# Kernel tuning notes

Hardware: AMD Instinct MI355X
Metric: run time of the kernel (lower is better)

## Reference

```python
import jax, jax.numpy as jnp
import numpy as np
import math

B, S, D, H = 2, 2048, 1024, 16
DH = D // H  # head_dim = 64
NEG = -10000.0


def setup_inputs() -> dict:
    key = jax.random.key(0)
    ks = jax.random.split(key, 6)
    scale = 1.0 / math.sqrt(D)
    inp = {
        "query": jax.random.normal(ks[0], (B, S, D), dtype=jnp.float32),
        "key": jax.random.normal(ks[1], (B, S, D), dtype=jnp.float32),
        "value": jax.random.normal(ks[2], (B, S, D), dtype=jnp.float32),
        "Wq": jax.random.normal(ks[3], (D, D), dtype=jnp.float32) * scale,
        "Wk": jax.random.normal(ks[4], (D, D), dtype=jnp.float32) * scale,
        "Wv": jax.random.normal(ks[5], (D, D), dtype=jnp.float32) * scale,
        "pad_mask": jnp.ones((B, 1, 1, S), dtype=jnp.int32),
        "attn_mask": jnp.tril(jnp.ones((S, S), dtype=jnp.int32))[None, None],  # causal [1,1,S,S]
    }
    return inp


def reference(query, key, value, Wq, Wk, Wv, pad_mask, attn_mask):
    b, s, d = query.shape
    # torch Linear(bias=False): y = x @ W.T ; then split into heads [B,H,S,DH]
    def proj(x, W):
        return (x @ W.T).reshape(b, -1, H, DH).transpose(0, 2, 1, 3)

    Q = proj(query, Wq)
    K = proj(key, Wk)
    V = proj(value, Wv)

    scores = jnp.einsum("bhqd,bhkd->bhqk", Q, K) / math.sqrt(DH)
    scores = jnp.where(attn_mask == 0, NEG, scores)
    scores = jnp.where(pad_mask == 0, NEG, scores)
    attn = jax.nn.softmax(scores, axis=-1)  # dropout p=0.0 -> identity
    ctx = jnp.einsum("bhqk,bhkd->bhqd", attn, V)
    return ctx.transpose(0, 2, 1, 3).reshape(b, -1, d)
```

## Files before the change

### kernel.cpp

```cpp
#include <hip/hip_runtime.h>


typedef unsigned short u16;
typedef unsigned int u32;
typedef u16 u16x4 __attribute__((ext_vector_type(4)));
typedef u16 u16x8 __attribute__((ext_vector_type(8)));
typedef u32 u32x2 __attribute__((ext_vector_type(2)));
typedef u32 u32x4 __attribute__((ext_vector_type(4)));
typedef __bf16 bf16x8 __attribute__((ext_vector_type(8)));
typedef float f32x4 __attribute__((ext_vector_type(4)));

static __device__ __forceinline__ u16 f2bf(float f) {
  unsigned u = __builtin_bit_cast(unsigned, f);
  return (u16)((u + 0x7FFFu + ((u >> 16) & 1u)) >> 16);
}

static __device__ __forceinline__ u32 cvt_pk_bf16(float lo, float hi) {
  u32 r;
  asm("v_cvt_pk_bf16_f32 %0, %1, %2" : "=v"(r) : "v"(lo), "v"(hi));
  return r;
}

static __device__ __forceinline__ u16x8 cvt8(float4 f0, float4 f1) {
  u32x4 v;
  v[0] = cvt_pk_bf16(f0.x, f0.y);
  v[1] = cvt_pk_bf16(f0.z, f0.w);
  v[2] = cvt_pk_bf16(f1.x, f1.y);
  v[3] = cvt_pk_bf16(f1.z, f1.w);
  return __builtin_bit_cast(u16x8, v);
}

static __device__ __forceinline__ f32x4 mfma16(u16x8 a, u16x8 b, f32x4 c) {
  return __builtin_amdgcn_mfma_f32_16x16x32_bf16(
      __builtin_bit_cast(bf16x8, a), __builtin_bit_cast(bf16x8, b), c, 0, 0, 0);
}

static __device__ __forceinline__ float bperm_f(int lane, float v) {
  return __builtin_bit_cast(
      float, __builtin_amdgcn_ds_bpermute(lane * 4, __builtin_bit_cast(int, v)));
}

#define GLOAD16(GSRC, LDST)                                                  \
  __builtin_amdgcn_global_load_lds(                                         \
      (const __attribute__((address_space(1))) unsigned int*)(GSRC),        \
      (__attribute__((address_space(3))) unsigned int*)(LDST), 16, 0, 0)

#define FENCE() asm volatile("" ::: "memory")
#define BARX()                        \
  do {                                \
    __builtin_amdgcn_s_barrier();     \
    FENCE();                          \
  } while (0)

__global__ __launch_bounds__(256) void cvt_kernel(
    const float* __restrict__ Xq, const float* __restrict__ Xk,
    const float* __restrict__ Xv, const float* __restrict__ Wq,
    const float* __restrict__ Wk, const float* __restrict__ Wv,
    u16* __restrict__ Xb, u16* __restrict__ Wb) {
  const int y = blockIdx.y;
  const float* src = (y == 0) ? Xq : (y == 1) ? Xk : (y == 2) ? Xv
                   : (y == 3) ? Wq : (y == 4) ? Wk : Wv;
  const size_t nelem = (y < 3) ? (size_t)4 * 1024 * 1024 : (size_t)1024 * 1024;
  u16* dst = (y < 3) ? Xb + (size_t)y * 4 * 1024 * 1024
                     : Wb + (size_t)(y - 3) * 1024 * 1024;
  const size_t i = ((size_t)blockIdx.x * 256 + threadIdx.x) * 8;
  if (i >= nelem) return;
  const float4 f0 = *(const float4*)(src + i);
  const float4 f1 = *(const float4*)(src + i + 4);
  *(u16x8*)(dst + i) = cvt8(f0, f1);
}

__global__ __launch_bounds__(256) void proj_kernel(
    const u16* __restrict__ Xbf, const u16* __restrict__ Wbf,
    u16* __restrict__ Qb, u16* __restrict__ Kb, u16* __restrict__ Vt) {
  const int d0 = blockIdx.x;
  const int tid = (d0 & 7) * 96 + (d0 >> 3);
  const int nI = tid % 24, mI = tid / 24;
  const int mode = nI >> 3;
  const int m0 = mI * 128;
  const int n0 = (nI & 7) * 128;

  const u16* __restrict__ X = Xbf + (size_t)mode * (4 * 1024 * 1024);
  const u16* __restrict__ W = Wbf + (size_t)mode * (1024 * 1024);

  __shared__ __align__(16) char As[3][128 * 64];
  __shared__ __align__(16) char Bs[3][128 * 64];

  const int t = threadIdx.x;
  const int lane = t & 63;
  const int w = t >> 6;
  const int wm = w >> 1, wn = w & 1;
  const int lr = lane & 15, lg = lane >> 4;

  const u16* aptr[2];
  const u16* bptr[2];
  int soff[2];
#pragma unroll
  for (int jj = 0; jj < 2; ++jj) {
    const int j = w * 2 + jj;
    const int row = j * 16 + (lane >> 2);
    const int col = (lane & 3) * 8;
    aptr[jj] = X + (size_t)(m0 + row) * 1024 + col;
    bptr[jj] = W + (size_t)(n0 + row) * 1024 + col;
    soff[jj] = j * 1024;
  }

#define ISSUE(T, BUF)                                                \
  do {                                                               \
    _Pragma("unroll") for (int jj = 0; jj < 2; ++jj)                 \
        GLOAD16(aptr[jj] + (size_t)(T) * 32, As[BUF] + soff[jj]);    \
    _Pragma("unroll") for (int jj = 0; jj < 2; ++jj)                 \
        GLOAD16(bptr[jj] + (size_t)(T) * 32, Bs[BUF] + soff[jj]);    \
  } while (0)

  f32x4 acc[4][4] = {};

#define CMP(BUF)                                                              \
  do {                                                                       \
    u16x8 af[4], bfr[4];                                                     \
    _Pragma("unroll") for (int mi = 0; mi < 4; ++mi) {                        \
      const int row = wm * 64 + mi * 16 + lr;                                \
      af[mi] = *(const u16x8*)(As[BUF] + row * 64 + lg * 16);                \
    }                                                                         \
    _Pragma("unroll") for (int ni = 0; ni < 4; ++ni) {                        \
      const int row = wn * 64 + ni * 16 + lr;                                \
      bfr[ni] = *(const u16x8*)(Bs[BUF] + row * 64 + lg * 16);               \
    }                                                                         \
    _Pragma("unroll") for (int mi = 0; mi < 4; ++mi)                          \
        _Pragma("unroll") for (int ni = 0; ni < 4; ++ni)                      \
            acc[mi][ni] = mfma16(af[mi], bfr[ni], acc[mi][ni]);               \
  } while (0)

  ISSUE(0, 0);
  ISSUE(1, 1);
  ISSUE(2, 2);
  asm volatile("s_waitcnt vmcnt(8)" ::: "memory");
  BARX();

  for (int tt = 0; tt < 29; ++tt) {
    CMP(tt % 3);
    asm volatile("s_waitcnt lgkmcnt(0)" ::: "memory");
    BARX();
    ISSUE(tt + 3, tt % 3);
    asm volatile("s_waitcnt vmcnt(8)" ::: "memory");
    BARX();
  }
  CMP(29 % 3);
  asm volatile("s_waitcnt vmcnt(4)" ::: "memory");
  BARX();
  CMP(30 % 3);
  asm volatile("s_waitcnt vmcnt(0)" ::: "memory");
  BARX();
  CMP(31 % 3);
#undef ISSUE
#undef CMP

#pragma unroll
  for (int mi = 0; mi < 4; ++mi) {
    const int sbase = m0 + wm * 64 + mi * 16 + lg * 4;
    const int b_ = sbase >> 11;
    const int s_ = sbase & 2047;
#pragma unroll
    for (int ni = 0; ni < 4; ++ni) {
      const int n = n0 + wn * 64 + ni * 16 + lr;
      const int h_ = n >> 6, dh = n & 63;
      if (mode == 2) {
        u16x4 pk;
        pk[0] = f2bf(acc[mi][ni][0]);
        pk[1] = f2bf(acc[mi][ni][1]);
        pk[2] = f2bf(acc[mi][ni][2]);
        pk[3] = f2bf(acc[mi][ni][3]);
        *(u16x4*)(Vt + ((size_t)((b_ * 16 + h_) * 64 + dh)) * 2048 + s_) = pk;
      } else {
        const float sc = (mode == 0) ? 0.18033688f : 1.0f;
        u16* dst = (mode == 0 ? Qb : Kb) + (size_t)(b_ * 16 + h_) * (2048 * 64) + dh;
#pragma unroll
        for (int r = 0; r < 4; ++r)
          dst[(size_t)(s_ + r) * 64] = f2bf(acc[mi][ni][r] * sc);
      }
    }
  }
}

__global__ __launch_bounds__(256, 2) void attn_kernel(
    const u16* __restrict__ Qb, const u16* __restrict__ Kb, const u16* __restrict__ Vt,
    const int* __restrict__ pad, float* __restrict__ out) {
  const int id = blockIdx.x;
  const int g = id >> 8, r_ = id & 255;
  const int bh = r_ & 31;
  const int p8 = r_ >> 5;
  const int pi = g ? (15 - p8) : p8;
  const int qbA = 31 - pi, qbB = pi;

  const int b = bh >> 4, h = bh & 15;
  const u16* Qh = Qb + (size_t)bh * (2048 * 64);
  const u16* Kh = Kb + (size_t)bh * (2048 * 64);
  const u16* Vh = Vt + (size_t)bh * (64 * 2048);
  const int* padb = pad + b * 2048;

  __shared__ u16 Ks[2][64 * 64];
  __shared__ u16 Vs[2][64 * 64];
  __shared__ u16 Ps[4][16 * 64];

  const int t = threadIdx.x, lane = t & 63, w = t >> 6;
  const int lr = lane & 15, lg = lane >> 4;
  const int swz = (lr & 7) << 4;
  const int sr = t >> 3, scb = t & 7;
  const int qwaveA = qbA * 64 + w * 16, qwaveB = qbB * 64 + w * 16;

  u16x8 qfA[2], qfB[2];
#pragma unroll
  for (int kc = 0; kc < 2; ++kc) {
    qfA[kc] = *(const u16x8*)(Qh + (size_t)(qwaveA + lr) * 64 + kc * 32 + lg * 8);
    qfB[kc] = *(const u16x8*)(Qh + (size_t)(qwaveB + lr) * 64 + kc * 32 + lg * 8);
  }

  f32x4 accA[4] = {}, accB[4] = {};
  float mrowA = -1e4f, lsumA = 0.f, mrowB = -1e4f, lsumB = 0.f;

  u16x8 kr0, kr1, vr0, vr1;
  const int sb0 = (sr * 128 + scb * 16) ^ ((sr & 7) << 4);
  const int sb1 = ((32 + sr) * 128 + scb * 16) ^ ((sr & 7) << 4);

  kr0 = *(const u16x8*)(Kh + (size_t)sr * 64 + scb * 8);
  kr1 = *(const u16x8*)(Kh + (size_t)(32 + sr) * 64 + scb * 8);
  vr0 = *(const u16x8*)(Vh + (size_t)sr * 2048 + scb * 8);
  vr1 = *(const u16x8*)(Vh + (size_t)(32 + sr) * 2048 + scb * 8);
  *(u16x8*)((char*)Ks[0] + sb0) = kr0;
  *(u16x8*)((char*)Ks[0] + sb1) = kr1;
  *(u16x8*)((char*)Vs[0] + sb0) = vr0;
  *(u16x8*)((char*)Vs[0] + sb1) = vr1;
  __syncthreads();

#define PROCESS(QF, ACC, MROW, LSUM, QWAVE)                                    \
  do {                                                                         \
    f32x4 s4[4] = {};                                                          \
    __builtin_amdgcn_s_setprio(1);                                             \
    _Pragma("unroll") for (int ct = 0; ct < 4; ++ct) {                         \
      if (kv0 + ct * 16 <= (QWAVE) + 15) {                                     \
        _Pragma("unroll") for (int kc = 0; kc < 2; ++kc) {                     \
          const int byt = ((ct * 16 + lr) * 128 + kc * 64 + lg * 16) ^ swz;    \
          const u16x8 kf = *(const u16x8*)((char*)KsC + byt);                  \
          s4[ct] = mfma16(kf, QF[kc], s4[ct]);                                 \
        }                                                                      \
      }                                                                        \
    }                                                                          \
    __builtin_amdgcn_s_setprio(0);                                             \
    float vv[4][4];                                                            \
    if ((kv0 + 63 <= (QWAVE)) && allpad) {                                     \
      _Pragma("unroll") for (int ct = 0; ct < 4; ++ct)                         \
          _Pragma("unroll") for (int rr = 0; rr < 4; ++rr)                     \
              vv[ct][rr] = s4[ct][rr];                                         \
    } else {                                                                   \
      const int lim = (QWAVE) + lr - kv0 - lg * 4;                             \
      _Pragma("unroll") for (int ct = 0; ct < 4; ++ct) {                       \
        const int* pvp = (const int*)&pv4[ct];                                 \
        _Pragma("unroll") for (int rr = 0; rr < 4; ++rr)                       \
            vv[ct][rr] = (pvp[rr] && (ct * 16 + rr) <= lim) ? s4[ct][rr]       \
                                                            : -1e4f;           \
      }                                                                        \
    }                                                                          \
    float m0_ = fmaxf(fmaxf(fmaxf(vv[0][0], vv[0][1]), fmaxf(vv[0][2], vv[0][3])), \
                      fmaxf(fmaxf(vv[1][0], vv[1][1]), fmaxf(vv[1][2], vv[1][3]))); \
    float m1_ = fmaxf(fmaxf(fmaxf(vv[2][0], vv[2][1]), fmaxf(vv[2][2], vv[2][3])), \
                      fmaxf(fmaxf(vv[3][0], vv[3][1]), fmaxf(vv[3][2], vv[3][3]))); \
    float mx = fmaxf(m0_, m1_);                                                \
    mx = fmaxf(mx, __shfl_xor(mx, 16));                                        \
    mx = fmaxf(mx, __shfl_xor(mx, 32));                                        \
    if (!__all(mx <= (MROW) + 8.0f)) { \
      const float mn = fmaxf((MROW), mx);                                      \
      const float al = exp2f((MROW) - mn);                                     \
      (MROW) = mn;                                                             \
      (LSUM) *= al;                                                            \
      _Pragma("unroll") for (int rr = 0; rr < 4; ++rr) {                       \
        const float alv = bperm_f(lg * 4 + rr, al);                            \
        _Pragma("unroll") for (int dt = 0; dt < 4; ++dt) ACC[dt][rr] *= alv;   \
      }                                                                        \
    }                                                                          \
    float p[4][4];                                                             \
    _Pragma("unroll") for (int ct = 0; ct < 4; ++ct)                           \
        _Pragma("unroll") for (int rr = 0; rr < 4; ++rr)                       \
            p[ct][rr] = exp2f(vv[ct][rr] - (MROW));                            \
    float ps = (((p[0][0] + p[0][1]) + (p[0][2] + p[0][3])) +                  \
                ((p[1][0] + p[1][1]) + (p[1][2] + p[1][3]))) +                 \
               (((p[2][0] + p[2][1]) + (p[2][2] + p[2][3])) +                  \
                ((p[3][0] + p[3][1]) + (p[3][2] + p[3][3])));                  \
    ps += __shfl_xor(ps, 16);                                                  \
    ps += __shfl_xor(ps, 32);                                                  \
    (LSUM) += ps;                                                              \
    u16* PsB = &Ps[w][0];                                                      \
    _Pragma("unroll") for (int ct = 0; ct < 4; ++ct) {                         \
      u32x2 pw;                                                                \
      pw[0] = cvt_pk_bf16(p[ct][0], p[ct][1]);                                 \
      pw[1] = cvt_pk_bf16(p[ct][2], p[ct][3]);                                 \
      const int pb = (lr * 128 + ct * 32 + lg * 8) ^ swz;                      \
      *(u32x2*)((char*)PsB + pb) = pw;                                         \
    }                                                                          \
    const u16x8 pa0 = *(const u16x8*)((char*)PsB + ((lr * 128 + lg * 16) ^ swz));      \
    const u16x8 pa1 = *(const u16x8*)((char*)PsB + ((lr * 128 + 64 + lg * 16) ^ swz)); \
    __builtin_amdgcn_s_setprio(1);                                             \
    _Pragma("unroll") for (int dt = 0; dt < 4; ++dt) {                         \
      const int r0 = (dt * 16 + lr) * 128;                                     \
      ACC[dt] = mfma16(pa0, *(const u16x8*)((char*)VsC + ((r0 + lg * 16) ^ swz)), ACC[dt]);      \
      ACC[dt] = mfma16(pa1, *(const u16x8*)((char*)VsC + ((r0 + 64 + lg * 16) ^ swz)), ACC[dt]); \
    }                                                                          \
    __builtin_amdgcn_s_setprio(0);                                             \
  } while (0)

  int cur = 0;
  const int nst = qbA + 1;
  for (int st = 0; st < nst; ++st) {
    const int kv0 = st << 6;
    const bool more = st + 1 < nst;
    if (more) {
      const int nv0 = kv0 + 64;
      kr0 = *(const u16x8*)(Kh + (size_t)(nv0 + sr) * 64 + scb * 8);
      kr1 = *(const u16x8*)(Kh + (size_t)(nv0 + 32 + sr) * 64 + scb * 8);
      vr0 = *(const u16x8*)(Vh + (size_t)sr * 2048 + nv0 + scb * 8);
      vr1 = *(const u16x8*)(Vh + (size_t)(32 + sr) * 2048 + nv0 + scb * 8);
    }
    int4 pv4[4];
#pragma unroll
    for (int ct = 0; ct < 4; ++ct)
      pv4[ct] = *(const int4*)(padb + kv0 + ct * 16 + lg * 4);
    const int pall = pv4[0].x & pv4[0].y & pv4[0].z & pv4[0].w &
                     pv4[1].x & pv4[1].y & pv4[1].z & pv4[1].w &
                     pv4[2].x & pv4[2].y & pv4[2].z & pv4[2].w &
                     pv4[3].x & pv4[3].y & pv4[3].z & pv4[3].w;
    const bool allpad = __all(pall != 0);

    const u16* KsC = Ks[cur];
    const u16* VsC = Vs[cur];

    PROCESS(qfA, accA, mrowA, lsumA, qwaveA);
    if (st <= qbB)
      PROCESS(qfB, accB, mrowB, lsumB, qwaveB);

    if (more) {
      u16* Kn = Ks[cur ^ 1];
      u16* Vn = Vs[cur ^ 1];
      *(u16x8*)((char*)Kn + sb0) = kr0;
      *(u16x8*)((char*)Kn + sb1) = kr1;
      *(u16x8*)((char*)Vn + sb0) = vr0;
      *(u16x8*)((char*)Vn + sb1) = vr1;
    }
    __syncthreads();
    cur ^= 1;
  }
#undef PROCESS

#pragma unroll
  for (int tile = 0; tile < 2; ++tile) {
    const f32x4* acc = tile ? accB : accA;
    const float lsum = tile ? lsumB : lsumA;
    const int qwave = tile ? qwaveB : qwaveA;
    const float il = 1.0f / lsum;
    float* obase = out + ((size_t)(b * 2048 + qwave + lg * 4)) * 1024 + h * 64 + lr;
#pragma unroll
    for (int r = 0; r < 4; ++r) {
      const float linv = bperm_f(lg * 4 + r, il);
#pragma unroll
      for (int dt = 0; dt < 4; ++dt)
        obase[(size_t)r * 1024 + dt * 16] = acc[dt][r] * linv;
    }
  }
}

extern "C" void kernel_launch(void* const* d_in, const int* in_sizes, int n_in,
                              void* d_out, int out_size, void* d_ws, size_t ws_size,
                              hipStream_t stream) {
  const float* q  = (const float*)d_in[0];
  const float* k  = (const float*)d_in[1];
  const float* v  = (const float*)d_in[2];
  const float* wq = (const float*)d_in[3];
  const float* wk = (const float*)d_in[4];
  const float* wv = (const float*)d_in[5];
  const int* pad  = (const int*)d_in[6];
  float* out = (float*)d_out;

  u16* Qb  = (u16*)d_ws;
  u16* Kb  = Qb + (size_t)4 * 1024 * 1024;
  u16* Vt  = Kb + (size_t)4 * 1024 * 1024;
  u16* Wbf = Vt + (size_t)4 * 1024 * 1024;
  u16* Xbf = Wbf + (size_t)3 * 1024 * 1024;

  dim3 gv(2048, 6);
  cvt_kernel<<<gv, 256, 0, stream>>>(q, k, v, wq, wk, wv, Xbf, Wbf);

  proj_kernel<<<768, 256, 0, stream>>>(Xbf, Wbf, Qb, Kb, Vt);

  attn_kernel<<<512, 256, 0, stream>>>(Qb, Kb, Vt, pad, out);
}
```

Measured before the change: 106.0 us.

## Assign each wave 32 rows of one query tile, sharing K/V fragments

Work is split differently across waves. Before, each wave handled 16 rows of both query tiles. Now waves 0-1 take 32 rows of tile A and waves 2-3 take 32 rows of tile B, processing two 16-row groups together. Each K and V fragment read from LDS then feeds two MFMAs, roughly halving LDS traffic per unit of work, and the P scratch buffer doubles to 8 slices. The cost is load imbalance under the causal mask: the tile-B waves go idle once their tile is finished, while the tile-A waves carry double work on the critical path.

```diff
diff --git a/kernel.cpp b/kernel.cpp
--- a/kernel.cpp
+++ b/kernel.cpp
@@ -200,23 +200,26 @@
 
   __shared__ u16 Ks[2][64 * 64];
   __shared__ u16 Vs[2][64 * 64];
-  __shared__ u16 Ps[4][16 * 64];
+  __shared__ u16 Ps[8][16 * 64];
 
   const int t = threadIdx.x, lane = t & 63, w = t >> 6;
   const int lr = lane & 15, lg = lane >> 4;
   const int swz = (lr & 7) << 4;
   const int sr = t >> 3, scb = t & 7;
-  const int qwaveA = qbA * 64 + w * 16, qwaveB = qbB * 64 + w * 16;
-
-  u16x8 qfA[2], qfB[2];
-#pragma unroll
-  for (int kc = 0; kc < 2; ++kc) {
-    qfA[kc] = *(const u16x8*)(Qh + (size_t)(qwaveA + lr) * 64 + kc * 32 + lg * 8);
-    qfB[kc] = *(const u16x8*)(Qh + (size_t)(qwaveB + lr) * 64 + kc * 32 + lg * 8);
-  }
-
-  f32x4 accA[4] = {}, accB[4] = {};
-  float mrowA = -1e4f, lsumA = 0.f, mrowB = -1e4f, lsumB = 0.f;
+
+  const int myqb = (w >> 1) ? qbB : qbA;
+  const int qwave = myqb * 64 + (w & 1) * 32;
+
+  u16x8 qf[2][2];
+#pragma unroll
+  for (int gp = 0; gp < 2; ++gp)
+#pragma unroll
+    for (int kc = 0; kc < 2; ++kc)
+      qf[gp][kc] =
+          *(const u16x8*)(Qh + (size_t)(qwave + gp * 16 + lr) * 64 + kc * 32 + lg * 8);
+
+  f32x4 acc[2][4] = {};
+  float mrow[2] = {-1e4f, -1e4f}, lsum[2] = {0.f, 0.f};
 
   u16x8 kr0, kr1, vr0, vr1;
   const int sb0 = (sr * 128 + scb * 16) ^ ((sr & 7) << 4);
@@ -231,81 +234,6 @@
   *(u16x8*)((char*)Vs[0] + sb0) = vr0;
   *(u16x8*)((char*)Vs[0] + sb1) = vr1;
   __syncthreads();
-
-#define PROCESS(QF, ACC, MROW, LSUM, QWAVE)                                    \
-  do {                                                                         \
-    f32x4 s4[4] = {};                                                          \
-    __builtin_amdgcn_s_setprio(1);                                             \
-    _Pragma("unroll") for (int ct = 0; ct < 4; ++ct) {                         \
-      if (kv0 + ct * 16 <= (QWAVE) + 15) {                                     \
-        _Pragma("unroll") for (int kc = 0; kc < 2; ++kc) {                     \
-          const int byt = ((ct * 16 + lr) * 128 + kc * 64 + lg * 16) ^ swz;    \
-          const u16x8 kf = *(const u16x8*)((char*)KsC + byt);                  \
-          s4[ct] = mfma16(kf, QF[kc], s4[ct]);                                 \
-        }                                                                      \
-      }                                                                        \
-    }                                                                          \
-    __builtin_amdgcn_s_setprio(0);                                             \
-    float vv[4][4];                                                            \
-    if ((kv0 + 63 <= (QWAVE)) && allpad) {                                     \
-      _Pragma("unroll") for (int ct = 0; ct < 4; ++ct)                         \
-          _Pragma("unroll") for (int rr = 0; rr < 4; ++rr)                     \
-              vv[ct][rr] = s4[ct][rr];                                         \
-    } else {                                                                   \
-      const int lim = (QWAVE) + lr - kv0 - lg * 4;                             \
-      _Pragma("unroll") for (int ct = 0; ct < 4; ++ct) {                       \
-        const int* pvp = (const int*)&pv4[ct];                                 \
-        _Pragma("unroll") for (int rr = 0; rr < 4; ++rr)                       \
-            vv[ct][rr] = (pvp[rr] && (ct * 16 + rr) <= lim) ? s4[ct][rr]       \
-                                                            : -1e4f;           \
-      }                                                                        \
-    }                                                                          \
-    float m0_ = fmaxf(fmaxf(fmaxf(vv[0][0], vv[0][1]), fmaxf(vv[0][2], vv[0][3])), \
-                      fmaxf(fmaxf(vv[1][0], vv[1][1]), fmaxf(vv[1][2], vv[1][3]))); \
-    float m1_ = fmaxf(fmaxf(fmaxf(vv[2][0], vv[2][1]), fmaxf(vv[2][2], vv[2][3])), \
-                      fmaxf(fmaxf(vv[3][0], vv[3][1]), fmaxf(vv[3][2], vv[3][3]))); \
-    float mx = fmaxf(m0_, m1_);                                                \
-    mx = fmaxf(mx, __shfl_xor(mx, 16));                                        \
-    mx = fmaxf(mx, __shfl_xor(mx, 32));                                        \
-    if (!__all(mx <= (MROW) + 8.0f)) { \
-      const float mn = fmaxf((MROW), mx);                                      \
-      const float al = exp2f((MROW) - mn);                                     \
-      (MROW) = mn;                                                             \
-      (LSUM) *= al;                                                            \
-      _Pragma("unroll") for (int rr = 0; rr < 4; ++rr) {                       \
-        const float alv = bperm_f(lg * 4 + rr, al);                            \
-        _Pragma("unroll") for (int dt = 0; dt < 4; ++dt) ACC[dt][rr] *= alv;   \
-      }                                                                        \
-    }                                                                          \
-    float p[4][4];                                                             \
-    _Pragma("unroll") for (int ct = 0; ct < 4; ++ct)                           \
-        _Pragma("unroll") for (int rr = 0; rr < 4; ++rr)                       \
-            p[ct][rr] = exp2f(vv[ct][rr] - (MROW));                            \
-    float ps = (((p[0][0] + p[0][1]) + (p[0][2] + p[0][3])) +                  \
-                ((p[1][0] + p[1][1]) + (p[1][2] + p[1][3]))) +                 \
-               (((p[2][0] + p[2][1]) + (p[2][2] + p[2][3])) +                  \
-                ((p[3][0] + p[3][1]) + (p[3][2] + p[3][3])));                  \
-    ps += __shfl_xor(ps, 16);                                                  \
-    ps += __shfl_xor(ps, 32);                                                  \
-    (LSUM) += ps;                                                              \
-    u16* PsB = &Ps[w][0];                                                      \
-    _Pragma("unroll") for (int ct = 0; ct < 4; ++ct) {                         \
-      u32x2 pw;                                                                \
-      pw[0] = cvt_pk_bf16(p[ct][0], p[ct][1]);                                 \
-      pw[1] = cvt_pk_bf16(p[ct][2], p[ct][3]);                                 \
-      const int pb = (lr * 128 + ct * 32 + lg * 8) ^ swz;                      \
-      *(u32x2*)((char*)PsB + pb) = pw;                                         \
-    }                                                                          \
-    const u16x8 pa0 = *(const u16x8*)((char*)PsB + ((lr * 128 + lg * 16) ^ swz));      \
-    const u16x8 pa1 = *(const u16x8*)((char*)PsB + ((lr * 128 + 64 + lg * 16) ^ swz)); \
-    __builtin_amdgcn_s_setprio(1);                                             \
-    _Pragma("unroll") for (int dt = 0; dt < 4; ++dt) {                         \
-      const int r0 = (dt * 16 + lr) * 128;                                     \
-      ACC[dt] = mfma16(pa0, *(const u16x8*)((char*)VsC + ((r0 + lg * 16) ^ swz)), ACC[dt]);      \
-      ACC[dt] = mfma16(pa1, *(const u16x8*)((char*)VsC + ((r0 + 64 + lg * 16) ^ swz)), ACC[dt]); \
-    }                                                                          \
-    __builtin_amdgcn_s_setprio(0);                                             \
-  } while (0)
 
   int cur = 0;
   const int nst = qbA + 1;
@@ -319,22 +247,144 @@
       vr0 = *(const u16x8*)(Vh + (size_t)sr * 2048 + nv0 + scb * 8);
       vr1 = *(const u16x8*)(Vh + (size_t)(32 + sr) * 2048 + nv0 + scb * 8);
     }
-    int4 pv4[4];
-#pragma unroll
-    for (int ct = 0; ct < 4; ++ct)
-      pv4[ct] = *(const int4*)(padb + kv0 + ct * 16 + lg * 4);
-    const int pall = pv4[0].x & pv4[0].y & pv4[0].z & pv4[0].w &
-                     pv4[1].x & pv4[1].y & pv4[1].z & pv4[1].w &
-                     pv4[2].x & pv4[2].y & pv4[2].z & pv4[2].w &
-                     pv4[3].x & pv4[3].y & pv4[3].z & pv4[3].w;
-    const bool allpad = __all(pall != 0);
-
-    const u16* KsC = Ks[cur];
-    const u16* VsC = Vs[cur];
-
-    PROCESS(qfA, accA, mrowA, lsumA, qwaveA);
-    if (st <= qbB)
-      PROCESS(qfB, accB, mrowB, lsumB, qwaveB);
+
+    if (st <= myqb) {
+      const u16* KsC = Ks[cur];
+      const u16* VsC = Vs[cur];
+
+      int4 pv4[4];
+#pragma unroll
+      for (int ct = 0; ct < 4; ++ct)
+        pv4[ct] = *(const int4*)(padb + kv0 + ct * 16 + lg * 4);
+      const int pall = pv4[0].x & pv4[0].y & pv4[0].z & pv4[0].w &
+                       pv4[1].x & pv4[1].y & pv4[1].z & pv4[1].w &
+                       pv4[2].x & pv4[2].y & pv4[2].z & pv4[2].w &
+                       pv4[3].x & pv4[3].y & pv4[3].z & pv4[3].w;
+      const bool allpad = __all(pall != 0);
+
+      f32x4 s4[2][4] = {};
+      __builtin_amdgcn_s_setprio(1);
+#pragma unroll
+      for (int ct = 0; ct < 4; ++ct) {
+        if (kv0 + ct * 16 <= qwave + 31) {
+#pragma unroll
+          for (int kc = 0; kc < 2; ++kc) {
+            const int byt = ((ct * 16 + lr) * 128 + kc * 64 + lg * 16) ^ swz;
+            const u16x8 kf = *(const u16x8*)((char*)KsC + byt);
+            s4[0][ct] = mfma16(kf, qf[0][kc], s4[0][ct]);
+            s4[1][ct] = mfma16(kf, qf[1][kc], s4[1][ct]);
+          }
+        }
+      }
+      __builtin_amdgcn_s_setprio(0);
+
+      float vv[2][4][4];
+#pragma unroll
+      for (int gp = 0; gp < 2; ++gp) {
+        if ((kv0 + 63 <= qwave + 16 * gp) && allpad) {
+#pragma unroll
+          for (int ct = 0; ct < 4; ++ct)
+#pragma unroll
+            for (int rr = 0; rr < 4; ++rr) vv[gp][ct][rr] = s4[gp][ct][rr];
+        } else {
+          const int lim = qwave + 16 * gp + lr - kv0 - lg * 4;
+#pragma unroll
+          for (int ct = 0; ct < 4; ++ct) {
+            const int* pvp = (const int*)&pv4[ct];
+#pragma unroll
+            for (int rr = 0; rr < 4; ++rr)
+              vv[gp][ct][rr] =
+                  (pvp[rr] && (ct * 16 + rr) <= lim) ? s4[gp][ct][rr] : -1e4f;
+          }
+        }
+      }
+
+      float mx[2];
+#pragma unroll
+      for (int gp = 0; gp < 2; ++gp) {
+        float a0 = fmaxf(fmaxf(fmaxf(vv[gp][0][0], vv[gp][0][1]),
+                               fmaxf(vv[gp][0][2], vv[gp][0][3])),
+                         fmaxf(fmaxf(vv[gp][1][0], vv[gp][1][1]),
+                               fmaxf(vv[gp][1][2], vv[gp][1][3])));
+        float a1 = fmaxf(fmaxf(fmaxf(vv[gp][2][0], vv[gp][2][1]),
+                               fmaxf(vv[gp][2][2], vv[gp][2][3])),
+                         fmaxf(fmaxf(vv[gp][3][0], vv[gp][3][1]),
+                               fmaxf(vv[gp][3][2], vv[gp][3][3])));
+        mx[gp] = fmaxf(a0, a1);
+      }
+      mx[0] = fmaxf(mx[0], __shfl_xor(mx[0], 16));
+      mx[1] = fmaxf(mx[1], __shfl_xor(mx[1], 16));
+      mx[0] = fmaxf(mx[0], __shfl_xor(mx[0], 32));
+      mx[1] = fmaxf(mx[1], __shfl_xor(mx[1], 32));
+
+#pragma unroll
+      for (int gp = 0; gp < 2; ++gp) {
+        if (!__all(mx[gp] <= mrow[gp] + 8.0f)) {
+          const float mn = fmaxf(mrow[gp], mx[gp]);
+          const float al = exp2f(mrow[gp] - mn);
+          mrow[gp] = mn;
+          lsum[gp] *= al;
+#pragma unroll
+          for (int rr = 0; rr < 4; ++rr) {
+            const float alv = bperm_f(lg * 4 + rr, al);
+#pragma unroll
+            for (int dt = 0; dt < 4; ++dt) acc[gp][dt][rr] *= alv;
+          }
+        }
+      }
+
+      float p[2][4][4];
+#pragma unroll
+      for (int gp = 0; gp < 2; ++gp)
+#pragma unroll
+        for (int ct = 0; ct < 4; ++ct)
+#pragma unroll
+          for (int rr = 0; rr < 4; ++rr)
+            p[gp][ct][rr] = exp2f(vv[gp][ct][rr] - mrow[gp]);
+
+      float ps[2];
+#pragma unroll
+      for (int gp = 0; gp < 2; ++gp)
+        ps[gp] = ((((p[gp][0][0] + p[gp][0][1]) + (p[gp][0][2] + p[gp][0][3])) +
+                   ((p[gp][1][0] + p[gp][1][1]) + (p[gp][1][2] + p[gp][1][3]))) +
+                  (((p[gp][2][0] + p[gp][2][1]) + (p[gp][2][2] + p[gp][2][3])) +
+                   ((p[gp][3][0] + p[gp][3][1]) + (p[gp][3][2] + p[gp][3][3]))));
+      ps[0] += __shfl_xor(ps[0], 16);
+      ps[1] += __shfl_xor(ps[1], 16);
+      ps[0] += __shfl_xor(ps[0], 32);
+      ps[1] += __shfl_xor(ps[1], 32);
+      lsum[0] += ps[0];
+      lsum[1] += ps[1];
+
+      u16x8 pa0[2], pa1[2];
+#pragma unroll
+      for (int gp = 0; gp < 2; ++gp) {
+        u16* PsB = &Ps[w * 2 + gp][0];
+#pragma unroll
+        for (int ct = 0; ct < 4; ++ct) {
+          u32x2 pw;
+          pw[0] = cvt_pk_bf16(p[gp][ct][0], p[gp][ct][1]);
+          pw[1] = cvt_pk_bf16(p[gp][ct][2], p[gp][ct][3]);
+          const int pb = (lr * 128 + ct * 32 + lg * 8) ^ swz;
+          *(u32x2*)((char*)PsB + pb) = pw;
+        }
+        pa0[gp] = *(const u16x8*)((char*)PsB + ((lr * 128 + lg * 16) ^ swz));
+        pa1[gp] = *(const u16x8*)((char*)PsB + ((lr * 128 + 64 + lg * 16) ^ swz));
+      }
+
+      __builtin_amdgcn_s_setprio(1);
+#pragma unroll
+      for (int dt = 0; dt < 4; ++dt) {
+        const int r0 = (dt * 16 + lr) * 128;
+        const u16x8 vf0 = *(const u16x8*)((char*)VsC + ((r0 + lg * 16) ^ swz));
+        const u16x8 vf1 = *(const u16x8*)((char*)VsC + ((r0 + 64 + lg * 16) ^ swz));
+        acc[0][dt] = mfma16(pa0[0], vf0, acc[0][dt]);
+        acc[1][dt] = mfma16(pa0[1], vf0, acc[1][dt]);
+        acc[0][dt] = mfma16(pa1[0], vf1, acc[0][dt]);
+        acc[1][dt] = mfma16(pa1[1], vf1, acc[1][dt]);
+      }
+      __builtin_amdgcn_s_setprio(0);
+    }
 
     if (more) {
       u16* Kn = Ks[cur ^ 1];
@@ -347,21 +397,18 @@
     __syncthreads();
     cur ^= 1;
   }
-#undef PROCESS
-
-#pragma unroll
-  for (int tile = 0; tile < 2; ++tile) {
-    const f32x4* acc = tile ? accB : accA;
-    const float lsum = tile ? lsumB : lsumA;
-    const int qwave = tile ? qwaveB : qwaveA;
-    const float il = 1.0f / lsum;
-    float* obase = out + ((size_t)(b * 2048 + qwave + lg * 4)) * 1024 + h * 64 + lr;
+
+#pragma unroll
+  for (int gp = 0; gp < 2; ++gp) {
+    const float il = 1.0f / lsum[gp];
+    float* obase =
+        out + ((size_t)(b * 2048 + qwave + gp * 16 + lg * 4)) * 1024 + h * 64 + lr;
 #pragma unroll
     for (int r = 0; r < 4; ++r) {
       const float linv = bperm_f(lg * 4 + r, il);
 #pragma unroll
       for (int dt = 0; dt < 4; ++dt)
-        obase[(size_t)r * 1024 + dt * 16] = acc[dt][r] * linv;
+        obase[(size_t)r * 1024 + dt * 16] = acc[gp][dt][r] * linv;
     }
   }
 }
```

After: 125.3 us. +18.2%, slower.
